# Performance work log

Measured on AMD Instinct MI355X. Metric: run time of the kernel, lower is better.

## Reference

```python
import jax, jax.numpy as jnp
import numpy as np

B, T, N_EMBD, HEAD = 4, 4096, 2048, 128


def setup_inputs() -> dict:
    key = jax.random.key(0)
    kx, kq, kk, kv = jax.random.split(key, 4)
    scale = 1.0 / np.sqrt(N_EMBD)
    return {
        "x": jax.random.normal(kx, (B, T, N_EMBD), dtype=jnp.float32),
        "Wq": jax.random.normal(kq, (N_EMBD, HEAD), dtype=jnp.float32) * scale,
        "Wk": jax.random.normal(kk, (N_EMBD, HEAD), dtype=jnp.float32) * scale,
        "Wv": jax.random.normal(kv, (N_EMBD, HEAD), dtype=jnp.float32) * scale,
    }


def reference(x, Wq, Wk, Wv):
    # q, k, v: [B, T, H]
    q = jnp.einsum("btn,nh->bth", x, Wq)
    k = jnp.einsum("btn,nh->bth", x, Wk)
    v = jnp.einsum("btn,nh->bth", x, Wv)
    scale = 1.0 / jnp.sqrt(jnp.asarray(HEAD, dtype=x.dtype))
    scores = jnp.einsum("bth,bsh->bts", q, k) * scale  # [B, T, T]
    causal = jnp.tril(jnp.ones((T, T), dtype=bool))
    scores = jnp.where(causal, scores, -jnp.inf)
    weights = jax.nn.softmax(scores, axis=-1)  # dropout p=0.0 -> identity
    return jnp.einsum("bts,bsh->bth", weights, v)
```

## Files before the change

### kernel.cpp

```cpp
#include <hip/hip_runtime.h>
#include <hip/hip_bf16.h>

#define B_SZ  4
#define T_SEQ 4096
#define NE    2048
#define HD    128
#define NROWS (B_SZ * T_SEQ)

typedef __attribute__((ext_vector_type(4))) float f32x4;
typedef __attribute__((ext_vector_type(8))) short s16x8;

__device__ __forceinline__ ushort f2bf(float f) {
    __hip_bfloat16 h = __float2bfloat16(f);
    return *reinterpret_cast<ushort*>(&h);
}
__device__ __forceinline__ unsigned int pk2(float a, float b) {
    return (unsigned int)f2bf(a) | ((unsigned int)f2bf(b) << 16);
}
__device__ __forceinline__ void gload_lds16(const void* g, void* l) {
    __builtin_amdgcn_global_load_lds(
        (const __attribute__((address_space(1))) unsigned int*)g,
        (__attribute__((address_space(3))) unsigned int*)l, 16, 0, 0);
}

__global__ __launch_bounds__(256) void wconv_kernel(
    const float* __restrict__ Wq, const float* __restrict__ Wk,
    const float* __restrict__ Wv, ushort* __restrict__ wt)
{
    __shared__ __align__(16) ushort tr[128][80];
    const int mat = blockIdx.y;
    const int k0  = blockIdx.x * 64;
    const float* W = (mat == 0) ? Wq : (mat == 1) ? Wk : Wv;
    const int tid = threadIdx.x;

    #pragma unroll
    for (int p = 0; p < 32; p++) {
        const int idx = p * 256 + tid;
        const int k = idx >> 7, h = idx & 127;
        tr[h][k] = f2bf(W[(size_t)(k0 + k) * HD + h]);
    }
    __syncthreads();
    const int h = tid >> 1, half = tid & 1;
    const uint4* src = (const uint4*)&tr[h][half * 32];
    uint4* dst = (uint4*)(wt + (size_t)(mat * HD + h) * NE + k0 + half * 32);
    #pragma unroll
    for (int j = 0; j < 4; j++) dst[j] = src[j];
}

__global__ __launch_bounds__(256) void qkv_kernel(
    const float* __restrict__ x, const ushort* __restrict__ wt,
    ushort* __restrict__ q_b, ushort* __restrict__ k_b, ushort* __restrict__ vt)
{
    __shared__ __align__(16) ushort xa[2][32][32];
    __shared__ __align__(16) ushort wb[2][384][32];

    const int tid  = threadIdx.x;
    const int wave = tid >> 6, lane = tid & 63;
    const int nn   = lane & 15, quad = lane >> 4;
    const int rows0 = blockIdx.x * 32;
    const int mrow  = (wave & 1) * 16;
    const int wc    = (wave >> 1) * 192;

    f32x4 acc[12];
    #pragma unroll
    for (int nt = 0; nt < 12; nt++) acc[nt] = (f32x4){0.f, 0.f, 0.f, 0.f};

    const int xrow = tid >> 3, xk = (tid & 7) * 4;
    const float* xp = x + (size_t)(rows0 + xrow) * NE + xk;
    float4 xr;
    auto load_x = [&](int kc) { xr = *(const float4*)(xp + kc); };
    auto write_x = [&](int buf) {
        uint2 w;
        w.x = pk2(xr.x, xr.y);
        w.y = pk2(xr.z, xr.w);
        *(uint2*)&xa[buf][xrow][xk] = w;
    };

    const char* wsrc0 = (const char*)wt + (size_t)(tid >> 2) * (NE * 2) + (tid & 3) * 16;
    char* wdst0 = (char*)wb + tid * 16;
    auto stage_w = [&](int buf, int kc) {
        #pragma unroll
        for (int rnd = 0; rnd < 6; rnd++)
            gload_lds16(wsrc0 + (size_t)rnd * 64 * (NE * 2) + kc * 2,
                        wdst0 + buf * 24576 + rnd * 4096);
    };

    load_x(0);
    stage_w(0, 0);
    write_x(0);
    asm volatile("s_waitcnt vmcnt(0)" ::: "memory");
    __syncthreads();

    for (int t = 0; t < 64; t++) {
        const int cb = t & 1;
        if (t + 1 < 64) { load_x((t + 1) * 32); stage_w(cb ^ 1, (t + 1) * 32); }
        const s16x8 af = *(const s16x8*)&xa[cb][mrow + nn][quad * 8];
        #pragma unroll
        for (int nt = 0; nt < 12; nt++) {
            const s16x8 bf = *(const s16x8*)&wb[cb][wc + nt * 16 + nn][quad * 8];
            acc[nt] = __builtin_amdgcn_mfma_f32_16x16x32_bf16(af, bf, acc[nt], 0, 0, 0);
        }
        if (t + 1 < 64) write_x(cb ^ 1);
        __syncthreads();
    }

    const float qscale = 0.08838834764831845f;
    #pragma unroll
    for (int nt = 0; nt < 12; nt++) {
        const int c = wc + nt * 16 + nn;
        #pragma unroll
        for (int r = 0; r < 4; r++) {
            const int grow = rows0 + mrow + quad * 4 + r;
            const float val = acc[nt][r];
            if (c < 128)       q_b[(size_t)grow * HD + c] = f2bf(val * qscale);
            else if (c < 256)  k_b[(size_t)grow * HD + (c - 128)] = f2bf(val);
            else               vt[(size_t)(c - 256) * NROWS + grow] = f2bf(val);
        }
    }
}

__global__ __launch_bounds__(256) void attn_kernel(
    const ushort* __restrict__ q_b, const ushort* __restrict__ k_b,
    const ushort* __restrict__ vt, float* __restrict__ out)
{
    __shared__ __align__(16) char smem_raw[4 * 32 * 132 * 4];
    float (*o_smem)[32][132] = reinterpret_cast<float (*)[32][132]>(smem_raw);
    ushort (*pT)[68]         = reinterpret_cast<ushort (*)[68]>(smem_raw);
    __shared__ float l_smem[4][32];

    const int bid = blockIdx.x;
    const int xcd = bid & 7;
    const int b   = xcd >> 1;
    const int qi  = 127 - (((bid >> 3) << 1) | (xcd & 1));
    const int qrow0 = qi * 32;
    const size_t bT = (size_t)b * T_SEQ;

    const int tid  = threadIdx.x;
    const int wave = tid >> 6, lane = tid & 63;
    const int nn   = lane & 15, quad = lane >> 4;

    s16x8 qfrag[2][4];
    #pragma unroll
    for (int m = 0; m < 2; m++)
        #pragma unroll
        for (int ks = 0; ks < 4; ks++)
            qfrag[m][ks] = *(const s16x8*)&q_b[(bT + qrow0 + m * 16 + nn) * HD + ks * 32 + quad * 8];

    s16x8 ones;
    #pragma unroll
    for (int j = 0; j < 8; j++) ones[j] = (short)0x3F80;

    f32x4 o_acc[2][8], l_acc[2];
    #pragma unroll
    for (int m = 0; m < 2; m++) {
        #pragma unroll
        for (int nt = 0; nt < 8; nt++) o_acc[m][nt] = (f32x4){0.f, 0.f, 0.f, 0.f};
        l_acc[m] = (f32x4){0.f, 0.f, 0.f, 0.f};
    }

    const int ntiles = (qi >> 1) + 1;

    for (int t = wave; t < ntiles; t += 4) {
        const int s0 = t * 64;
        const bool lastt = (t == ntiles - 1);

        s16x8 kf[4][4];
        #pragma unroll
        for (int ks = 0; ks < 4; ks++)
            #pragma unroll
            for (int n = 0; n < 4; n++)
                kf[ks][n] = *(const s16x8*)&k_b[(bT + s0 + n * 16 + nn) * HD + ks * 32 + quad * 8];

        f32x4 sa[2][4];
        #pragma unroll
        for (int m = 0; m < 2; m++)
            #pragma unroll
            for (int n = 0; n < 4; n++) sa[m][n] = (f32x4){0.f, 0.f, 0.f, 0.f};
        #pragma unroll
        for (int ks = 0; ks < 4; ks++)
            #pragma unroll
            for (int n = 0; n < 4; n++)
                #pragma unroll
                for (int m = 0; m < 2; m++)
                    sa[m][n] = __builtin_amdgcn_mfma_f32_16x16x32_bf16(
                        qfrag[m][ks], kf[ks][n], sa[m][n], 0, 0, 0);

        s16x8 vb[8][2];
        #pragma unroll
        for (int nt = 0; nt < 8; nt++)
            #pragma unroll
            for (int kst = 0; kst < 2; kst++)
                vb[nt][kst] = *(const s16x8*)&vt[(size_t)(nt * 16 + nn) * NROWS + bT + s0 + kst * 32 + quad * 8];

        #pragma unroll
        for (int m = 0; m < 2; m++)
            #pragma unroll
            for (int r = 0; r < 4; r++) {
                const int grow = qrow0 + m * 16 + quad * 4 + r;
                #pragma unroll
                for (int n = 0; n < 4; n++) {
                    const float p = (lastt && (s0 + n * 16 + nn > grow)) ? 0.0f : __expf(sa[m][n][r]);
                    pT[wave * 32 + m * 16 + quad * 4 + r][n * 16 + nn] = f2bf(p);
                }
            }

        s16x8 pf[2][2];
        #pragma unroll
        for (int m = 0; m < 2; m++)
            #pragma unroll
            for (int kst = 0; kst < 2; kst++)
                pf[m][kst] = *(const s16x8*)&pT[wave * 32 + m * 16 + nn][kst * 32 + quad * 8];

        #pragma unroll
        for (int m = 0; m < 2; m++)
            #pragma unroll
            for (int kst = 0; kst < 2; kst++)
                l_acc[m] = __builtin_amdgcn_mfma_f32_16x16x32_bf16(pf[m][kst], ones, l_acc[m], 0, 0, 0);

        #pragma unroll
        for (int nt = 0; nt < 8; nt++)
            #pragma unroll
            for (int kst = 0; kst < 2; kst++)
                #pragma unroll
                for (int m = 0; m < 2; m++)
                    o_acc[m][nt] = __builtin_amdgcn_mfma_f32_16x16x32_bf16(
                        pf[m][kst], vb[nt][kst], o_acc[m][nt], 0, 0, 0);
    }

    __syncthreads();

    #pragma unroll
    for (int m = 0; m < 2; m++) {
        if (nn == 0) {
            #pragma unroll
            for (int r = 0; r < 4; r++)
                l_smem[wave][m * 16 + quad * 4 + r] = l_acc[m][r];
        }
        #pragma unroll
        for (int nt = 0; nt < 8; nt++)
            #pragma unroll
            for (int r = 0; r < 4; r++)
                o_smem[wave][m * 16 + quad * 4 + r][nt * 16 + nn] = o_acc[m][nt][r];
    }

    __syncthreads();

    #pragma unroll
    for (int half = 0; half < 2; half++)
        #pragma unroll
        for (int rr = 0; rr < 4; rr++) {
            const int row = half * 16 + quad * 4 + rr;
            const float L = l_smem[0][row] + l_smem[1][row] + l_smem[2][row] + l_smem[3][row];
            const float invL = 1.0f / L;
            #pragma unroll
            for (int j = 0; j < 2; j++) {
                const int col = wave * 32 + j * 16 + nn;
                float s = 0.0f;
                #pragma unroll
                for (int p = 0; p < 4; p++) s += o_smem[p][row][col];
                out[(bT + qrow0 + row) * HD + col] = s * invL;
            }
        }
}

extern "C" void kernel_launch(void* const* d_in, const int* in_sizes, int n_in,
                              void* d_out, int out_size, void* d_ws, size_t ws_size,
                              hipStream_t stream) {
    const float* x  = (const float*)d_in[0];
    const float* Wq = (const float*)d_in[1];
    const float* Wk = (const float*)d_in[2];
    const float* Wv = (const float*)d_in[3];

    ushort* q_b = (ushort*)d_ws;
    ushort* k_b = q_b + (size_t)NROWS * HD;
    ushort* vtp = k_b + (size_t)NROWS * HD;
    ushort* wt  = vtp + (size_t)HD * NROWS;

    wconv_kernel<<<dim3(32, 3), dim3(256), 0, stream>>>(Wq, Wk, Wv, wt);
    qkv_kernel<<<dim3(512), dim3(256), 0, stream>>>(x, wt, q_b, k_b, vtp);
    attn_kernel<<<dim3(512), dim3(256), 0, stream>>>(q_b, k_b, vtp, (float*)d_out);
}
```

Baseline: 334.1 us.

## Drop LDS staging in QKV projection, load operands directly with 64-row tiles

The QKV projection kernel no longer double-buffers x and weight tiles through shared memory with barriers. Each wave now loads its x rows and weight fragments straight from global memory into registers and computes a 32x192 block. The tile grows to 64 rows per block, so the grid halves to 256 blocks. This removes LDS traffic and __syncthreads but gives up software prefetch, raises register pressure (launch bounds set to 1 block), and makes global reads less coalesced, with weights re-read per wave from L2. The attention kernel's transposed-P LDS row pitch is also padded from 68 to 72 elements, apparently to change bank conflicts or alignment.

```diff
diff --git a/kernel.cpp b/kernel.cpp
--- a/kernel.cpp
+++ b/kernel.cpp
@@ -16,11 +16,6 @@
 }
 __device__ __forceinline__ unsigned int pk2(float a, float b) {
     return (unsigned int)f2bf(a) | ((unsigned int)f2bf(b) << 16);
-}
-__device__ __forceinline__ void gload_lds16(const void* g, void* l) {
-    __builtin_amdgcn_global_load_lds(
-        (const __attribute__((address_space(1))) unsigned int*)g,
-        (__attribute__((address_space(3))) unsigned int*)l, 16, 0, 0);
 }
 
 __global__ __launch_bounds__(256) void wconv_kernel(
@@ -47,76 +42,75 @@
     for (int j = 0; j < 4; j++) dst[j] = src[j];
 }
 
-__global__ __launch_bounds__(256) void qkv_kernel(
+__global__ __launch_bounds__(256, 1) void qkv_kernel(
     const float* __restrict__ x, const ushort* __restrict__ wt,
     ushort* __restrict__ q_b, ushort* __restrict__ k_b, ushort* __restrict__ vt)
 {
-    __shared__ __align__(16) ushort xa[2][32][32];
-    __shared__ __align__(16) ushort wb[2][384][32];
-
     const int tid  = threadIdx.x;
     const int wave = tid >> 6, lane = tid & 63;
     const int nn   = lane & 15, quad = lane >> 4;
-    const int rows0 = blockIdx.x * 32;
-    const int mrow  = (wave & 1) * 16;
-    const int wc    = (wave >> 1) * 192;
-
-    f32x4 acc[12];
-    #pragma unroll
-    for (int nt = 0; nt < 12; nt++) acc[nt] = (f32x4){0.f, 0.f, 0.f, 0.f};
-
-    const int xrow = tid >> 3, xk = (tid & 7) * 4;
-    const float* xp = x + (size_t)(rows0 + xrow) * NE + xk;
-    float4 xr;
-    auto load_x = [&](int kc) { xr = *(const float4*)(xp + kc); };
-    auto write_x = [&](int buf) {
-        uint2 w;
-        w.x = pk2(xr.x, xr.y);
-        w.y = pk2(xr.z, xr.w);
-        *(uint2*)&xa[buf][xrow][xk] = w;
-    };
-
-    const char* wsrc0 = (const char*)wt + (size_t)(tid >> 2) * (NE * 2) + (tid & 3) * 16;
-    char* wdst0 = (char*)wb + tid * 16;
-    auto stage_w = [&](int buf, int kc) {
-        #pragma unroll
-        for (int rnd = 0; rnd < 6; rnd++)
-            gload_lds16(wsrc0 + (size_t)rnd * 64 * (NE * 2) + kc * 2,
-                        wdst0 + buf * 24576 + rnd * 4096);
-    };
-
-    load_x(0);
-    stage_w(0, 0);
-    write_x(0);
-    asm volatile("s_waitcnt vmcnt(0)" ::: "memory");
-    __syncthreads();
+    const int rows0 = blockIdx.x * 64;
+    const int wm    = (wave >> 1) * 32;
+    const int wc    = (wave & 1) * 192;
+
+    f32x4 acc[2][12];
+    #pragma unroll
+    for (int m = 0; m < 2; m++)
+        #pragma unroll
+        for (int nt = 0; nt < 12; nt++) acc[m][nt] = (f32x4){0.f, 0.f, 0.f, 0.f};
+
+    const float*  xp0 = x  + (size_t)(rows0 + wm + nn) * NE + quad * 8;
+    const float*  xp1 = xp0 + (size_t)16 * NE;
+    const ushort* wp  = wt + (size_t)(wc + nn) * NE + quad * 8;
 
     for (int t = 0; t < 64; t++) {
-        const int cb = t & 1;
-        if (t + 1 < 64) { load_x((t + 1) * 32); stage_w(cb ^ 1, (t + 1) * 32); }
-        const s16x8 af = *(const s16x8*)&xa[cb][mrow + nn][quad * 8];
+        const int kc = t * 32;
+
+        const float4 a00 = *(const float4*)(xp0 + kc);
+        const float4 a01 = *(const float4*)(xp0 + kc + 4);
+        const float4 a10 = *(const float4*)(xp1 + kc);
+        const float4 a11 = *(const float4*)(xp1 + kc + 4);
+
+        s16x8 bf[12];
+        #pragma unroll
+        for (int nt = 0; nt < 12; nt++)
+            bf[nt] = *(const s16x8*)(wp + (size_t)nt * 16 * NE + kc);
+
+        s16x8 af[2];
+        {
+            uint4 w;
+            w.x = pk2(a00.x, a00.y); w.y = pk2(a00.z, a00.w);
+            w.z = pk2(a01.x, a01.y); w.w = pk2(a01.z, a01.w);
+            af[0] = *reinterpret_cast<s16x8*>(&w);
+            uint4 v;
+            v.x = pk2(a10.x, a10.y); v.y = pk2(a10.z, a10.w);
+            v.z = pk2(a11.x, a11.y); v.w = pk2(a11.z, a11.w);
+            af[1] = *reinterpret_cast<s16x8*>(&v);
+        }
+
+        #pragma unroll
+        for (int nt = 0; nt < 12; nt++)
+            #pragma unroll
+            for (int m = 0; m < 2; m++)
+                acc[m][nt] = __builtin_amdgcn_mfma_f32_16x16x32_bf16(
+                    af[m], bf[nt], acc[m][nt], 0, 0, 0);
+    }
+
+    const float qscale = 0.08838834764831845f;
+    #pragma unroll
+    for (int m = 0; m < 2; m++)
         #pragma unroll
         for (int nt = 0; nt < 12; nt++) {
-            const s16x8 bf = *(const s16x8*)&wb[cb][wc + nt * 16 + nn][quad * 8];
-            acc[nt] = __builtin_amdgcn_mfma_f32_16x16x32_bf16(af, bf, acc[nt], 0, 0, 0);
-        }
-        if (t + 1 < 64) write_x(cb ^ 1);
-        __syncthreads();
-    }
-
-    const float qscale = 0.08838834764831845f;
-    #pragma unroll
-    for (int nt = 0; nt < 12; nt++) {
-        const int c = wc + nt * 16 + nn;
-        #pragma unroll
-        for (int r = 0; r < 4; r++) {
-            const int grow = rows0 + mrow + quad * 4 + r;
-            const float val = acc[nt][r];
-            if (c < 128)       q_b[(size_t)grow * HD + c] = f2bf(val * qscale);
-            else if (c < 256)  k_b[(size_t)grow * HD + (c - 128)] = f2bf(val);
-            else               vt[(size_t)(c - 256) * NROWS + grow] = f2bf(val);
-        }
-    }
+            const int c = wc + nt * 16 + nn;
+            #pragma unroll
+            for (int r = 0; r < 4; r++) {
+                const int grow = rows0 + wm + m * 16 + quad * 4 + r;
+                const float val = acc[m][nt][r];
+                if (c < 128)       q_b[(size_t)grow * HD + c] = f2bf(val * qscale);
+                else if (c < 256)  k_b[(size_t)grow * HD + (c - 128)] = f2bf(val);
+                else               vt[(size_t)(c - 256) * NROWS + grow] = f2bf(val);
+            }
+        }
 }
 
 __global__ __launch_bounds__(256) void attn_kernel(
@@ -125,7 +119,7 @@
 {
     __shared__ __align__(16) char smem_raw[4 * 32 * 132 * 4];
     float (*o_smem)[32][132] = reinterpret_cast<float (*)[32][132]>(smem_raw);
-    ushort (*pT)[68]         = reinterpret_cast<ushort (*)[68]>(smem_raw);
+    ushort (*pT)[72]         = reinterpret_cast<ushort (*)[72]>(smem_raw);
     __shared__ float l_smem[4][32];
 
     const int bid = blockIdx.x;
@@ -277,6 +271,6 @@
     ushort* wt  = vtp + (size_t)HD * NROWS;
 
     wconv_kernel<<<dim3(32, 3), dim3(256), 0, stream>>>(Wq, Wk, Wv, wt);
-    qkv_kernel<<<dim3(512), dim3(256), 0, stream>>>(x, wt, q_b, k_b, vtp);
+    qkv_kernel<<<dim3(256), dim3(256), 0, stream>>>(x, wt, q_b, k_b, vtp);
     attn_kernel<<<dim3(512), dim3(256), 0, stream>>>(q_b, k_b, vtp, (float*)d_out);
 }
```

Measured after the change: 378.1 us. +13.2%, slower.
